# Kernel tuning notes

Hardware: AMD Instinct MI355X
Metric: run time of the kernel (lower is better)

Reference implementation:

```python
import jax, jax.numpy as jnp
import numpy as np

N = 50000      # nodes
E = 800000     # edges
D_IN = 128     # input feature dim
HID = 64       # out_channels (per-head dim; concat=False -> head mean)
HEADS = 2
NEG_SLOPE = 0.2


def gat_layer(x, src, dst, Ws, Wd, a_s, a_d, b):
    # PyG GATConv, add_self_loops=False, concat=False (mean over heads)
    n = x.shape[0]
    H, C = a_s.shape
    hs = (x @ Ws).reshape(n, H, C)          # source-side features [N,H,C]
    hd = (x @ Wd).reshape(n, H, C)          # dest-side features   [N,H,C]
    als = (hs * a_s).sum(-1)                # [N,H]
    ald = (hd * a_d).sum(-1)                # [N,H]
    e = jax.nn.leaky_relu(als[src] + ald[dst], NEG_SLOPE)   # [E,H]
    # segment softmax over edges grouped by destination node
    m = jax.ops.segment_max(e, dst, num_segments=n)
    m = jax.lax.stop_gradient(jnp.where(jnp.isfinite(m), m, 0.0))
    ex = jnp.exp(e - m[dst])
    den = jax.ops.segment_sum(ex, dst, num_segments=n)
    alpha = ex / (den[dst] + 1e-16)                          # [E,H]
    out = jax.ops.segment_sum(hs[src] * alpha[:, :, None], dst, num_segments=n)
    return out.mean(axis=1) + b             # [N,C]


def setup_inputs() -> dict:
    key = jax.random.key(0)
    ks = jax.random.split(key, 32)
    d = {}
    d["x"] = jax.random.normal(ks[0], (N, D_IN), jnp.float32)
    d["edge_index"] = jax.random.randint(ks[1], (2, E), 0, N, jnp.int32)
    dins = [D_IN, HID, HID]
    i = 2
    for l in range(1, 4):
        din = dins[l - 1]
        s = 1.0 / np.sqrt(din)
        d[f"Ws{l}"] = jax.random.normal(ks[i], (din, HEADS * HID), jnp.float32) * s; i += 1
        d[f"Wd{l}"] = jax.random.normal(ks[i], (din, HEADS * HID), jnp.float32) * s; i += 1
        d[f"as{l}"] = jax.random.normal(ks[i], (HEADS, HID), jnp.float32) * 0.1; i += 1
        d[f"ad{l}"] = jax.random.normal(ks[i], (HEADS, HID), jnp.float32) * 0.1; i += 1
        d[f"b{l}"] = jnp.zeros((HID,), jnp.float32)
        d[f"Wl{l}"] = jax.random.normal(ks[i], (din, HID), jnp.float32) * s; i += 1
        d[f"bl{l}"] = jnp.zeros((HID,), jnp.float32)
    return d


def reference(x, edge_index,
              Ws1, Wd1, as1, ad1, b1, Wl1, bl1,
              Ws2, Wd2, as2, ad2, b2, Wl2, bl2,
              Ws3, Wd3, as3, ad3, b3, Wl3, bl3):
    src, dst = edge_index[0], edge_index[1]
    h = jax.nn.relu(gat_layer(x, src, dst, Ws1, Wd1, as1, ad1, b1) + x @ Wl1 + bl1)
    h = jax.nn.relu(gat_layer(h, src, dst, Ws2, Wd2, as2, ad2, b2) + h @ Wl2 + bl2)
    h = jax.nn.relu(gat_layer(h, src, dst, Ws3, Wd3, as3, ad3, b3) + h @ Wl3 + bl3)
    return h
```

## Files before the change

### kernel.cpp

```cpp
#include <hip/hip_runtime.h>
#include <hip/hip_bf16.h>

#define NN 50000
#define NE 800000
#define SCAN_BS 1024
#define SCAN_NB ((NN + SCAN_BS - 1) / SCAN_BS)
#define EB ((NE + 255) / 256)
#define GB ((NN + 63) / 64)
#define RB ((NN + 1 + 255) / 256)

typedef __attribute__((ext_vector_type(8))) __bf16 bf16x8;
typedef __attribute__((ext_vector_type(4))) float float4v;

__device__ __forceinline__ unsigned pack_bf2(float lo, float hi) {
    union { __bf16 b; unsigned short u; } a, c;
    a.b = (__bf16)lo; c.b = (__bf16)hi;
    return (unsigned)a.u | ((unsigned)c.u << 16);
}
__device__ __forceinline__ float2 unpack_bf2(unsigned v) {
    union { unsigned short u; __bf16 b; } lo, hi;
    lo.u = (unsigned short)(v & 0xffff); hi.u = (unsigned short)(v >> 16);
    return make_float2((float)lo.b, (float)hi.b);
}


__device__ __forceinline__ void convert_w_part(const float* __restrict__ Ws,
                                               const float* __restrict__ Wd,
                                               const float* __restrict__ Wl,
                                               __bf16* __restrict__ Wt, int NC, int i)
{
    if (i >= NC * 23040) return;
    int chunk = i / 23040, rem = i % 23040;
    int r = rem / 72, c = rem % 72;
    float v = 0.f;
    if (c < 64) {
        int k = chunk * 64 + c;
        if (r < 128)      v = Ws[k * 128 + r];
        else if (r < 256) v = Wd[k * 128 + (r - 128)];
        else              v = Wl[k * 64 + (r - 256)];
    }
    Wt[i] = (__bf16)v;
}

__global__ void __launch_bounds__(256)
prep_kernel(const int* __restrict__ ei, int* __restrict__ deg, int* __restrict__ rank,
            const float* __restrict__ Ws1, const float* __restrict__ Wd1,
            const float* __restrict__ Wl1, __bf16* __restrict__ Wt1,
            const float* __restrict__ Ws2, const float* __restrict__ Wd2,
            const float* __restrict__ Wl2, __bf16* __restrict__ Wt2,
            const float* __restrict__ Ws3, const float* __restrict__ Wd3,
            const float* __restrict__ Wl3, __bf16* __restrict__ Wt3)
{
    int bi = blockIdx.x;
    if (bi < EB) {
        int e = bi * 256 + threadIdx.x;
        if (e < NE) rank[e] = atomicAdd(&deg[ei[NE + e]], 1);
    } else if (bi < EB + 180) {
        convert_w_part(Ws1, Wd1, Wl1, Wt1, 2, (bi - EB) * 256 + threadIdx.x);
    } else if (bi < EB + 270) {
        convert_w_part(Ws2, Wd2, Wl2, Wt2, 1, (bi - EB - 180) * 256 + threadIdx.x);
    } else {
        convert_w_part(Ws3, Wd3, Wl3, Wt3, 1, (bi - EB - 270) * 256 + threadIdx.x);
    }
}


__global__ void __launch_bounds__(SCAN_BS)
scan12_kernel(const int* __restrict__ deg, int* __restrict__ exl,
              int* __restrict__ bsum, int* __restrict__ boff, int* __restrict__ ticket)
{
    __shared__ int sh[SCAN_BS];
    __shared__ int lastFlag;
    int t = threadIdx.x;
    int i = blockIdx.x * SCAN_BS + t;
    int v = (i < NN) ? deg[i] : 0;
    sh[t] = v;
    __syncthreads();
    for (int off = 1; off < SCAN_BS; off <<= 1) {
        int u = (t >= off) ? sh[t - off] : 0;
        __syncthreads();
        sh[t] += u;
        __syncthreads();
    }
    if (i < NN) exl[i] = sh[t] - v;
    if (t == SCAN_BS - 1) {
        bsum[blockIdx.x] = sh[t];
        __threadfence();
        lastFlag = (atomicAdd(ticket, 1) == SCAN_NB - 1);
    }
    __syncthreads();
    if (lastFlag && t < 64) {
        __threadfence();
        int l = t;
        int bv = (l < SCAN_NB) ? bsum[l] : 0;
        int own = bv;
        for (int off = 1; off < 64; off <<= 1) {
            int u = __shfl_up(bv, off);
            if (l >= off) bv += u;
        }
        if (l < SCAN_NB) boff[l] = bv - own;
    }
}


__device__ __forceinline__ bf16x8 load_af(const __bf16* p) { return *(const bf16x8*)p; }
__device__ __forceinline__ bf16x8 load_af(const float* p) {
    float4 u = *(const float4*)p;
    float4 v = *(const float4*)(p + 4);
    bf16x8 r;
    r[0] = (__bf16)u.x; r[1] = (__bf16)u.y; r[2] = (__bf16)u.z; r[3] = (__bf16)u.w;
    r[4] = (__bf16)v.x; r[5] = (__bf16)v.y; r[6] = (__bf16)v.z; r[7] = (__bf16)v.w;
    return r;
}

template <int K, typename TIN, bool FUSE>
__global__ void __launch_bounds__(256, 4)
mfma_gemm(const TIN* __restrict__ xin, const __bf16* __restrict__ Wt,
          const float* __restrict__ a_s, const float* __restrict__ a_d,
          unsigned* __restrict__ hsb, float* __restrict__ lin,
          float* __restrict__ als, float* __restrict__ ald,
          const int* __restrict__ ei, const int* __restrict__ rank,
          const int* __restrict__ exl, const int* __restrict__ boff,
          int* __restrict__ row, int* __restrict__ csr_src)
{
    const int tid = threadIdx.x;

    if (FUSE && blockIdx.x >= GB) {
        int bi = blockIdx.x - GB;
        if (bi < RB) {
            int i = bi * 256 + tid;
            if (i < NN)       row[i] = exl[i] + boff[i >> 10];
            else if (i == NN) row[i] = NE;
        } else {
            int e = (bi - RB) * 256 + tid;
            if (e < NE) {
                int s = ei[e], d = ei[NE + e];
                csr_src[exl[d] + boff[d >> 10] + rank[e]] = s;
            }
        }
        return;
    }

    constexpr int NPH = (K / 64) * 2;
    __shared__ __align__(16) char ldsW[160 * 144];

    const int lane = tid & 63;
    const int wave = tid >> 6;
    const int l15 = lane & 15, quad = lane >> 4;
    const int n0 = blockIdx.x * 64 + wave * 16;
    const int nA = min(n0 + l15, NN - 1);

    bf16x8 afr[K / 32];
#pragma unroll
    for (int ks = 0; ks < K / 32; ++ks)
        afr[ks] = load_af(xin + (size_t)nA * K + ks * 32 + quad * 8);

    const uint4* gW = (const uint4*)Wt;
    uint4* lw = (uint4*)ldsW;
    uint4 st[6];

#pragma unroll
    for (int i = 0; i < 6; ++i) { int idx = i * 256 + tid; if (idx < 1440) st[i] = gW[idx]; }

    float4v acc[20];
#pragma unroll
    for (int t = 0; t < 20; ++t) acc[t] = (float4v){0.f, 0.f, 0.f, 0.f};

#pragma unroll
    for (int ph = 0; ph < NPH; ++ph) {
        if (ph) __syncthreads();
#pragma unroll
        for (int i = 0; i < 6; ++i) { int idx = i * 256 + tid; if (idx < 1440) lw[idx] = st[i]; }
        __syncthreads();
        if (ph + 1 < NPH) {
            const uint4* gs = gW + (ph + 1) * 1440;
#pragma unroll
            for (int i = 0; i < 6; ++i) { int idx = i * 256 + tid; if (idx < 1440) st[i] = gs[idx]; }
        }
        const int hh = ph & 1, ch = ph >> 1;
#pragma unroll
        for (int ksh = 0; ksh < 2; ++ksh) {
#pragma unroll
            for (int tl = 0; tl < 10; ++tl) {
                bf16x8 bw = *(const bf16x8*)&ldsW[(tl * 16 + l15) * 144 + (ksh * 4 + quad) * 16];
                acc[hh * 10 + tl] =
                    __builtin_amdgcn_mfma_f32_16x16x32_bf16(bw, afr[ch * 2 + ksh], acc[hh * 10 + tl], 0, 0, 0);
            }
        }
    }

    float s0 = 0.f, s1 = 0.f, d0 = 0.f, d1 = 0.f;
#pragma unroll
    for (int t = 0; t < 4; ++t) {
        float4 as0 = *(const float4*)&a_s[t * 16 + quad * 4];
        float4 as1 = *(const float4*)&a_s[64 + t * 16 + quad * 4];
        float4 ad0 = *(const float4*)&a_d[t * 16 + quad * 4];
        float4 ad1 = *(const float4*)&a_d[64 + t * 16 + quad * 4];
        s0 += acc[t][0] * as0.x + acc[t][1] * as0.y + acc[t][2] * as0.z + acc[t][3] * as0.w;
        s1 += acc[t + 4][0] * as1.x + acc[t + 4][1] * as1.y + acc[t + 4][2] * as1.z + acc[t + 4][3] * as1.w;
        d0 += acc[t + 8][0] * ad0.x + acc[t + 8][1] * ad0.y + acc[t + 8][2] * ad0.z + acc[t + 8][3] * ad0.w;
        d1 += acc[t + 12][0] * ad1.x + acc[t + 12][1] * ad1.y + acc[t + 12][2] * ad1.z + acc[t + 12][3] * ad1.w;
    }
    s0 += __shfl_xor(s0, 16); s0 += __shfl_xor(s0, 32);
    s1 += __shfl_xor(s1, 16); s1 += __shfl_xor(s1, 32);
    d0 += __shfl_xor(d0, 16); d0 += __shfl_xor(d0, 32);
    d1 += __shfl_xor(d1, 16); d1 += __shfl_xor(d1, 32);

    int n = n0 + l15;
    if (n < NN) {
#pragma unroll
        for (int t = 0; t < 4; ++t) {
            uint4 u;
            u.x = pack_bf2(acc[t][0], acc[t + 4][0]);
            u.y = pack_bf2(acc[t][1], acc[t + 4][1]);
            u.z = pack_bf2(acc[t][2], acc[t + 4][2]);
            u.w = pack_bf2(acc[t][3], acc[t + 4][3]);
            *(uint4*)&hsb[(size_t)n * 64 + t * 16 + quad * 4] = u;
            *(float4*)&lin[(size_t)n * 64 + t * 16 + quad * 4] =
                make_float4(acc[16 + t][0], acc[16 + t][1], acc[16 + t][2], acc[16 + t][3]);
        }
        if (quad == 0) *(float2*)&als[(size_t)n * 2] = make_float2(s0, s1);
        if (quad == 1) *(float2*)&ald[(size_t)n * 2] = make_float2(d0, d1);
    }
}


__device__ __forceinline__ float2 edge_w(const float* __restrict__ als, int s,
                                         float ad0, float ad1)
{
    float2 al = *(const float2*)&als[s * 2];
    float e0 = al.x + ad0; e0 = (e0 >= 0.f) ? e0 : 0.2f * e0;
    float e1 = al.y + ad1; e1 = (e1 >= 0.f) ? e1 : 0.2f * e1;
    return make_float2(__expf(e0), __expf(e1));
}

__device__ __forceinline__ void store_q(float* p, float v0, float v1, float v2, float v3) {
    *(float4*)p = make_float4(v0, v1, v2, v3);
}
__device__ __forceinline__ void store_q(__bf16* p, float v0, float v1, float v2, float v3) {
    *(uint2*)p = make_uint2(pack_bf2(v0, v1), pack_bf2(v2, v3));
}

template <typename TO>
__global__ void __launch_bounds__(256, 8)
gat_aggregate(const int* __restrict__ row, const int* __restrict__ csr_src,
              const float* __restrict__ als, const float* __restrict__ ald,
              const unsigned* __restrict__ hsb, const float* __restrict__ lin,
              const float* __restrict__ b, const float* __restrict__ bl,
              TO* __restrict__ out)
{
    int w = (blockIdx.x * 256 + threadIdx.x) >> 6;
    int lane = threadIdx.x & 63;
    int q = lane >> 4;
    int l15 = lane & 15;
    if (w >= NN) return;
    int p0 = row[w], p1 = row[w + 1];
    float ad0 = ald[w * 2 + 0];
    float ad1 = ald[w * 2 + 1];

    float a0[4] = {0.f, 0.f, 0.f, 0.f};
    float a1[4] = {0.f, 0.f, 0.f, 0.f};
    float den0 = 0.f, den1 = 0.f;

    for (int p = p0 + q; p < p1; p += 16) {
#pragma unroll
        for (int j = 0; j < 4; ++j) {
            int pp = p + 4 * j;
            bool live = (pp < p1);
            int s = csr_src[live ? pp : p0];
            float2 e = edge_w(als, s, ad0, ad1);
            if (!live) e = make_float2(0.f, 0.f);
            uint4 g = *(const uint4*)&hsb[(size_t)s * 64 + 4 * l15];
            den0 += e.x; den1 += e.y;
            float2 h;
            h = unpack_bf2(g.x); a0[0] += e.x * h.x; a1[0] += e.y * h.y;
            h = unpack_bf2(g.y); a0[1] += e.x * h.x; a1[1] += e.y * h.y;
            h = unpack_bf2(g.z); a0[2] += e.x * h.x; a1[2] += e.y * h.y;
            h = unpack_bf2(g.w); a0[3] += e.x * h.x; a1[3] += e.y * h.y;
        }
    }

#pragma unroll
    for (int i = 0; i < 4; ++i) {
        a0[i] += __shfl_xor(a0[i], 16); a0[i] += __shfl_xor(a0[i], 32);
        a1[i] += __shfl_xor(a1[i], 16); a1[i] += __shfl_xor(a1[i], 32);
    }
    den0 += __shfl_xor(den0, 16); den0 += __shfl_xor(den0, 32);
    den1 += __shfl_xor(den1, 16); den1 += __shfl_xor(den1, 32);

    if (q == 0) {
        int c0 = 4 * l15;
        float r0 = 1.f / (den0 + 1e-16f);
        float r1 = 1.f / (den1 + 1e-16f);
        float4 lv = *(const float4*)&lin[(size_t)w * 64 + c0];
        float v0 = 0.5f * (a0[0] * r0 + a1[0] * r1) + b[c0 + 0] + bl[c0 + 0] + lv.x;
        float v1 = 0.5f * (a0[1] * r0 + a1[1] * r1) + b[c0 + 1] + bl[c0 + 1] + lv.y;
        float v2 = 0.5f * (a0[2] * r0 + a1[2] * r1) + b[c0 + 2] + bl[c0 + 2] + lv.z;
        float v3 = 0.5f * (a0[3] * r0 + a1[3] * r1) + b[c0 + 3] + bl[c0 + 3] + lv.w;
        store_q(&out[(size_t)w * 64 + c0],
                fmaxf(v0, 0.f), fmaxf(v1, 0.f), fmaxf(v2, 0.f), fmaxf(v3, 0.f));
    }
}


extern "C" void kernel_launch(void* const* d_in, const int* in_sizes, int n_in,
                              void* d_out, int out_size, void* d_ws, size_t ws_size,
                              hipStream_t stream)
{
    const float* x  = (const float*)d_in[0];
    const int*   ei = (const int*)d_in[1];
    const float* Ws[3]; const float* Wd[3]; const float* As[3]; const float* Ad[3];
    const float* Bb[3]; const float* Wl[3]; const float* Bl[3];
    for (int l = 0; l < 3; ++l) {
        int base = 2 + 7 * l;
        Ws[l] = (const float*)d_in[base + 0];
        Wd[l] = (const float*)d_in[base + 1];
        As[l] = (const float*)d_in[base + 2];
        Ad[l] = (const float*)d_in[base + 3];
        Bb[l] = (const float*)d_in[base + 4];
        Wl[l] = (const float*)d_in[base + 5];
        Bl[l] = (const float*)d_in[base + 6];
    }

    float* ws = (float*)d_ws;
    unsigned* hsb = (unsigned*)ws;
    float* lin  = (float*)(hsb + (size_t)NN * 64);
    float* als  = lin + (size_t)NN * 64;
    float* ald  = als + (size_t)NN * 2;
    __bf16* hb  = (__bf16*)(ald + (size_t)NN * 2);
    __bf16* Wt1 = hb + (size_t)NN * 64;
    __bf16* Wt2 = Wt1 + 2 * 320 * 72;
    __bf16* Wt3 = Wt2 + 320 * 72;
    int* row     = (int*)(Wt3 + 320 * 72);
    int* deg     = row + (NN + 1);
    int* ticket  = deg + NN;
    int* rank    = ticket + 1;
    int* exl     = rank + NE;
    int* bsum    = exl + NN;
    int* boff    = bsum + SCAN_NB;
    int* csr_src = boff + SCAN_NB;

    const int WB = (NN * 64 + 255) / 256;

    hipMemsetAsync(deg, 0, sizeof(int) * (NN + 1), stream);
    prep_kernel<<<EB + 360, 256, 0, stream>>>(ei, deg, rank,
        Ws[0], Wd[0], Wl[0], Wt1,
        Ws[1], Wd[1], Wl[1], Wt2,
        Ws[2], Wd[2], Wl[2], Wt3);
    scan12_kernel<<<SCAN_NB, SCAN_BS, 0, stream>>>(deg, exl, bsum, boff, ticket);

    for (int l = 0; l < 3; ++l) {
        if (l == 0) {
            mfma_gemm<128, float, true><<<GB + RB + EB, 256, 0, stream>>>(
                x, Wt1, As[0], Ad[0], hsb, lin, als, ald,
                ei, rank, exl, boff, row, csr_src);
        } else {
            const __bf16* wt = (l == 1) ? Wt2 : Wt3;
            mfma_gemm<64, __bf16, false><<<GB, 256, 0, stream>>>(
                hb, wt, As[l], Ad[l], hsb, lin, als, ald,
                nullptr, nullptr, nullptr, nullptr, nullptr, nullptr);
        }
        if (l == 2) {
            gat_aggregate<float><<<WB, 256, 0, stream>>>(
                row, csr_src, als, ald, hsb, lin, Bb[l], Bl[l], (float*)d_out);
        } else {
            gat_aggregate<__bf16><<<WB, 256, 0, stream>>>(
                row, csr_src, als, ald, hsb, lin, Bb[l], Bl[l], hb);
        }
    }
}
```

Before: 355.3 us.

## Fuse layer aggregation with next layer's MFMA GEMM via LDS tile

Layers 1 and 2 now run one kernel each: 64 destination nodes are aggregated per block, the ReLU'd bf16 result is written to LDS, and the next layer's projection GEMM (hs, lin, attention logits) runs directly from LDS. This removes the intermediate hb round-trip through global memory and two kernel launches, and ping-pongs the hs/lin/als/ald buffers. In exchange, aggregation now runs one wave per 16 nodes serially with a 4-blocks-per-SM bound, which lowers parallelism for the latency-bound gather phase.

```diff
diff --git a/kernel.cpp b/kernel.cpp
--- a/kernel.cpp
+++ b/kernel.cpp
@@ -240,6 +240,155 @@
 __device__ __forceinline__ void store_q(__bf16* p, float v0, float v1, float v2, float v3) {
     *(uint2*)p = make_uint2(pack_bf2(v0, v1), pack_bf2(v2, v3));
 }
+
+__global__ void __launch_bounds__(256, 4)
+fused_agg_gemm(const int* __restrict__ row, const int* __restrict__ csr_src,
+               const float* __restrict__ alsP, const float* __restrict__ aldP,
+               const unsigned* __restrict__ hsbP, const float* __restrict__ linP,
+               const float* __restrict__ bP, const float* __restrict__ blP,
+               const __bf16* __restrict__ Wt,
+               const float* __restrict__ a_s, const float* __restrict__ a_d,
+               unsigned* __restrict__ hsbQ, float* __restrict__ linQ,
+               float* __restrict__ alsQ, float* __restrict__ aldQ)
+{
+    __shared__ __align__(16) char ldsW[160 * 144];
+    __shared__ __align__(16) char h_lds[64 * 144];
+
+    const int tid  = threadIdx.x;
+    const int lane = tid & 63;
+    const int wave = tid >> 6;
+    const int q    = lane >> 4;
+    const int l15  = lane & 15;
+    const int nblk = blockIdx.x * 64;
+
+    {
+        uint4* hz = (uint4*)h_lds;
+        for (int i = tid; i < 576; i += 256) hz[i] = (uint4){0u, 0u, 0u, 0u};
+    }
+    __syncthreads();
+
+    for (int i = 0; i < 16; ++i) {
+        int w = nblk + wave * 16 + i;
+        if (w >= NN) break;
+        int p0 = row[w], p1 = row[w + 1];
+        float ad0 = aldP[w * 2 + 0];
+        float ad1 = aldP[w * 2 + 1];
+        float a0[4] = {0.f, 0.f, 0.f, 0.f};
+        float a1[4] = {0.f, 0.f, 0.f, 0.f};
+        float den0 = 0.f, den1 = 0.f;
+
+        for (int p = p0 + q; p < p1; p += 16) {
+#pragma unroll
+            for (int j = 0; j < 4; ++j) {
+                int pp = p + 4 * j;
+                bool live = (pp < p1);
+                int s = csr_src[live ? pp : p0];
+                float2 e = edge_w(alsP, s, ad0, ad1);
+                if (!live) e = make_float2(0.f, 0.f);
+                uint4 g = *(const uint4*)&hsbP[(size_t)s * 64 + 4 * l15];
+                den0 += e.x; den1 += e.y;
+                float2 h;
+                h = unpack_bf2(g.x); a0[0] += e.x * h.x; a1[0] += e.y * h.y;
+                h = unpack_bf2(g.y); a0[1] += e.x * h.x; a1[1] += e.y * h.y;
+                h = unpack_bf2(g.z); a0[2] += e.x * h.x; a1[2] += e.y * h.y;
+                h = unpack_bf2(g.w); a0[3] += e.x * h.x; a1[3] += e.y * h.y;
+            }
+        }
+#pragma unroll
+        for (int k = 0; k < 4; ++k) {
+            a0[k] += __shfl_xor(a0[k], 16); a0[k] += __shfl_xor(a0[k], 32);
+            a1[k] += __shfl_xor(a1[k], 16); a1[k] += __shfl_xor(a1[k], 32);
+        }
+        den0 += __shfl_xor(den0, 16); den0 += __shfl_xor(den0, 32);
+        den1 += __shfl_xor(den1, 16); den1 += __shfl_xor(den1, 32);
+
+        if (q == 0) {
+            int c0 = 4 * l15;
+            float r0 = 1.f / (den0 + 1e-16f);
+            float r1 = 1.f / (den1 + 1e-16f);
+            float4 lv = *(const float4*)&linP[(size_t)w * 64 + c0];
+            float v0 = fmaxf(0.5f * (a0[0] * r0 + a1[0] * r1) + bP[c0 + 0] + blP[c0 + 0] + lv.x, 0.f);
+            float v1 = fmaxf(0.5f * (a0[1] * r0 + a1[1] * r1) + bP[c0 + 1] + blP[c0 + 1] + lv.y, 0.f);
+            float v2 = fmaxf(0.5f * (a0[2] * r0 + a1[2] * r1) + bP[c0 + 2] + blP[c0 + 2] + lv.z, 0.f);
+            float v3 = fmaxf(0.5f * (a0[3] * r0 + a1[3] * r1) + bP[c0 + 3] + blP[c0 + 3] + lv.w, 0.f);
+            int slot = wave * 16 + i;
+            *(uint2*)&h_lds[slot * 144 + 8 * l15] =
+                make_uint2(pack_bf2(v0, v1), pack_bf2(v2, v3));
+        }
+    }
+    __syncthreads();
+
+    bf16x8 afr[2];
+    afr[0] = *(const bf16x8*)&h_lds[(wave * 16 + l15) * 144 + 0  + q * 16];
+    afr[1] = *(const bf16x8*)&h_lds[(wave * 16 + l15) * 144 + 64 + q * 16];
+
+    const uint4* gW = (const uint4*)Wt;
+    uint4* lw = (uint4*)ldsW;
+    uint4 st[6];
+#pragma unroll
+    for (int i = 0; i < 6; ++i) { int idx = i * 256 + tid; if (idx < 1440) st[i] = gW[idx]; }
+
+    float4v acc[20];
+#pragma unroll
+    for (int t = 0; t < 20; ++t) acc[t] = (float4v){0.f, 0.f, 0.f, 0.f};
+
+#pragma unroll
+    for (int ph = 0; ph < 2; ++ph) {
+        if (ph) __syncthreads();
+#pragma unroll
+        for (int i = 0; i < 6; ++i) { int idx = i * 256 + tid; if (idx < 1440) lw[idx] = st[i]; }
+        __syncthreads();
+        if (ph == 0) {
+            const uint4* gs = gW + 1440;
+#pragma unroll
+            for (int i = 0; i < 6; ++i) { int idx = i * 256 + tid; if (idx < 1440) st[i] = gs[idx]; }
+        }
+#pragma unroll
+        for (int ksh = 0; ksh < 2; ++ksh) {
+#pragma unroll
+            for (int tl = 0; tl < 10; ++tl) {
+                bf16x8 bw = *(const bf16x8*)&ldsW[(tl * 16 + l15) * 144 + (ksh * 4 + q) * 16];
+                acc[ph * 10 + tl] =
+                    __builtin_amdgcn_mfma_f32_16x16x32_bf16(bw, afr[ksh], acc[ph * 10 + tl], 0, 0, 0);
+            }
+        }
+    }
+
+    float s0 = 0.f, s1 = 0.f, d0 = 0.f, d1 = 0.f;
+#pragma unroll
+    for (int t = 0; t < 4; ++t) {
+        float4 as0 = *(const float4*)&a_s[t * 16 + q * 4];
+        float4 as1 = *(const float4*)&a_s[64 + t * 16 + q * 4];
+        float4 ad0 = *(const float4*)&a_d[t * 16 + q * 4];
+        float4 ad1 = *(const float4*)&a_d[64 + t * 16 + q * 4];
+        s0 += acc[t][0] * as0.x + acc[t][1] * as0.y + acc[t][2] * as0.z + acc[t][3] * as0.w;
+        s1 += acc[t + 4][0] * as1.x + acc[t + 4][1] * as1.y + acc[t + 4][2] * as1.z + acc[t + 4][3] * as1.w;
+        d0 += acc[t + 8][0] * ad0.x + acc[t + 8][1] * ad0.y + acc[t + 8][2] * ad0.z + acc[t + 8][3] * ad0.w;
+        d1 += acc[t + 12][0] * ad1.x + acc[t + 12][1] * ad1.y + acc[t + 12][2] * ad1.z + acc[t + 12][3] * ad1.w;
+    }
+    s0 += __shfl_xor(s0, 16); s0 += __shfl_xor(s0, 32);
+    s1 += __shfl_xor(s1, 16); s1 += __shfl_xor(s1, 32);
+    d0 += __shfl_xor(d0, 16); d0 += __shfl_xor(d0, 32);
+    d1 += __shfl_xor(d1, 16); d1 += __shfl_xor(d1, 32);
+
+    int n = nblk + wave * 16 + l15;
+    if (n < NN) {
+#pragma unroll
+        for (int t = 0; t < 4; ++t) {
+            uint4 u;
+            u.x = pack_bf2(acc[t][0], acc[t + 4][0]);
+            u.y = pack_bf2(acc[t][1], acc[t + 4][1]);
+            u.z = pack_bf2(acc[t][2], acc[t + 4][2]);
+            u.w = pack_bf2(acc[t][3], acc[t + 4][3]);
+            *(uint4*)&hsbQ[(size_t)n * 64 + t * 16 + q * 4] = u;
+            *(float4*)&linQ[(size_t)n * 64 + t * 16 + q * 4] =
+                make_float4(acc[16 + t][0], acc[16 + t][1], acc[16 + t][2], acc[16 + t][3]);
+        }
+        if (q == 0) *(float2*)&alsQ[(size_t)n * 2] = make_float2(s0, s1);
+        if (q == 1) *(float2*)&aldQ[(size_t)n * 2] = make_float2(d0, d1);
+    }
+}
+
 
 template <typename TO>
 __global__ void __launch_bounds__(256, 8)
@@ -323,12 +472,15 @@
     }
 
     float* ws = (float*)d_ws;
-    unsigned* hsb = (unsigned*)ws;
-    float* lin  = (float*)(hsb + (size_t)NN * 64);
-    float* als  = lin + (size_t)NN * 64;
-    float* ald  = als + (size_t)NN * 2;
-    __bf16* hb  = (__bf16*)(ald + (size_t)NN * 2);
-    __bf16* Wt1 = hb + (size_t)NN * 64;
+    unsigned* hsbA = (unsigned*)ws;
+    float* linA = (float*)(hsbA + (size_t)NN * 64);
+    unsigned* hsbB = (unsigned*)(linA + (size_t)NN * 64);
+    float* linB = (float*)(hsbB + (size_t)NN * 64);
+    float* alsA = linB + (size_t)NN * 64;
+    float* aldA = alsA + (size_t)NN * 2;
+    float* alsB = aldA + (size_t)NN * 2;
+    float* aldB = alsB + (size_t)NN * 2;
+    __bf16* Wt1 = (__bf16*)(aldB + (size_t)NN * 2);
     __bf16* Wt2 = Wt1 + 2 * 320 * 72;
     __bf16* Wt3 = Wt2 + 320 * 72;
     int* row     = (int*)(Wt3 + 320 * 72);
@@ -349,23 +501,18 @@
         Ws[2], Wd[2], Wl[2], Wt3);
     scan12_kernel<<<SCAN_NB, SCAN_BS, 0, stream>>>(deg, exl, bsum, boff, ticket);
 
-    for (int l = 0; l < 3; ++l) {
-        if (l == 0) {
-            mfma_gemm<128, float, true><<<GB + RB + EB, 256, 0, stream>>>(
-                x, Wt1, As[0], Ad[0], hsb, lin, als, ald,
-                ei, rank, exl, boff, row, csr_src);
-        } else {
-            const __bf16* wt = (l == 1) ? Wt2 : Wt3;
-            mfma_gemm<64, __bf16, false><<<GB, 256, 0, stream>>>(
-                hb, wt, As[l], Ad[l], hsb, lin, als, ald,
-                nullptr, nullptr, nullptr, nullptr, nullptr, nullptr);
-        }
-        if (l == 2) {
-            gat_aggregate<float><<<WB, 256, 0, stream>>>(
-                row, csr_src, als, ald, hsb, lin, Bb[l], Bl[l], (float*)d_out);
-        } else {
-            gat_aggregate<__bf16><<<WB, 256, 0, stream>>>(
-                row, csr_src, als, ald, hsb, lin, Bb[l], Bl[l], hb);
-        }
-    }
-}
+    mfma_gemm<128, float, true><<<GB + RB + EB, 256, 0, stream>>>(
+        x, Wt1, As[0], Ad[0], hsbA, linA, alsA, aldA,
+        ei, rank, exl, boff, row, csr_src);
+
+    fused_agg_gemm<<<GB, 256, 0, stream>>>(
+        row, csr_src, alsA, aldA, hsbA, linA, Bb[0], Bl[0],
+        Wt2, As[1], Ad[1], hsbB, linB, alsB, aldB);
+
+    fused_agg_gemm<<<GB, 256, 0, stream>>>(
+        row, csr_src, alsB, aldB, hsbB, linB, Bb[1], Bl[1],
+        Wt3, As[2], Ad[2], hsbA, linA, alsA, aldA);
+
+    gat_aggregate<float><<<WB, 256, 0, stream>>>(
+        row, csr_src, alsA, aldA, hsbA, linA, Bb[2], Bl[2], (float*)d_out);
+}
```

After: 388.6 us. 1.09x slower.
